# Performance work log

Measured on AMD Instinct MI355X. Metric: run time of the kernel, lower is better.

The kernel has to match this reference:

```python
import jax, jax.numpy as jnp
import numpy as np

N, IN_DIM, HID, HEADS, OUT_DIM = 50000, 128, 32, 4, 64
E, P = 800000, 500000
BN_EPS = 1e-5
NEG_SLOPE = 0.2


def setup_inputs() -> dict:
    key = jax.random.key(0)
    ks = jax.random.split(key, 16)
    inp = {
        "x": jax.random.normal(ks[0], (N, IN_DIM), jnp.float32),
        "ei": jax.random.randint(ks[1], (2, E), 0, N, jnp.int64),
        "src": jax.random.randint(ks[2], (P,), 0, N, jnp.int64),
        "dst": jax.random.randint(ks[3], (P,), 0, N, jnp.int64),
        # conv1: in_dim -> hidden, heads=4, concat
        "W1": jax.random.normal(ks[4], (IN_DIM, HEADS * HID), jnp.float32) * 0.1,
        "a1s": jax.random.normal(ks[5], (HEADS, HID), jnp.float32) * 0.1,
        "a1d": jax.random.normal(ks[6], (HEADS, HID), jnp.float32) * 0.1,
        "b1": jnp.zeros((HEADS * HID,), jnp.float32),
        "bn1_g": jnp.ones((HEADS * HID,), jnp.float32),
        "bn1_b": jnp.zeros((HEADS * HID,), jnp.float32),
        "bn1_m": jnp.zeros((HEADS * HID,), jnp.float32),
        "bn1_v": jnp.ones((HEADS * HID,), jnp.float32),
        # conv2: hidden*heads -> out_dim, heads=1, no concat
        "W2": jax.random.normal(ks[7], (HEADS * HID, OUT_DIM), jnp.float32) * 0.1,
        "a2s": jax.random.normal(ks[8], (1, OUT_DIM), jnp.float32) * 0.1,
        "a2d": jax.random.normal(ks[9], (1, OUT_DIM), jnp.float32) * 0.1,
        "b2": jnp.zeros((OUT_DIM,), jnp.float32),
        "bn2_g": jnp.ones((OUT_DIM,), jnp.float32),
        "bn2_b": jnp.zeros((OUT_DIM,), jnp.float32),
        "bn2_m": jnp.zeros((OUT_DIM,), jnp.float32),
        "bn2_v": jnp.ones((OUT_DIM,), jnp.float32),
        # head MLP: Linear(2*out_dim, out_dim) -> ELU -> Linear(out_dim, 1) -> Sigmoid
        "hW1": jax.random.normal(ks[10], (2 * OUT_DIM, OUT_DIM), jnp.float32) * 0.1,
        "hb1": jnp.zeros((OUT_DIM,), jnp.float32),
        "hW2": jax.random.normal(ks[11], (OUT_DIM, 1), jnp.float32) * 0.1,
        "hb2": jnp.zeros((1,), jnp.float32),
    }
    return inp


def gat_conv(x, e_src, e_dst, W, a_src, a_dst, bias, heads, out_dim, concat):
    # x: [N, F_in]; edges (with self-loops): e_src/e_dst [E']
    n = x.shape[0]
    h = (x @ W).reshape(n, heads, out_dim)            # [N, H, D]
    as_n = jnp.sum(h * a_src, axis=-1)                # [N, H]
    ad_n = jnp.sum(h * a_dst, axis=-1)                # [N, H]
    alpha = jax.nn.leaky_relu(as_n[e_src] + ad_n[e_dst], NEG_SLOPE)  # [E', H]
    # segment softmax over destination nodes
    m = jax.ops.segment_max(alpha, e_dst, num_segments=n)
    m = jnp.where(jnp.isfinite(m), m, 0.0)
    e = jnp.exp(alpha - m[e_dst])
    s = jax.ops.segment_sum(e, e_dst, num_segments=n)
    coef = e / (s[e_dst] + 1e-16)                     # [E', H]
    agg = jax.ops.segment_sum(h[e_src] * coef[:, :, None], e_dst, num_segments=n)
    out = agg.reshape(n, heads * out_dim) if concat else agg.mean(axis=1)
    return out + bias


def batch_norm(x, g, b, m, v):
    return (x - m) * jax.lax.rsqrt(v + BN_EPS) * g + b


def reference(x, ei, src, dst, W1, a1s, a1d, b1, bn1_g, bn1_b, bn1_m, bn1_v,
              W2, a2s, a2d, b2, bn2_g, bn2_b, bn2_m, bn2_v, hW1, hb1, hW2, hb2):
    n = x.shape[0]
    # PyG GATConv default add_self_loops=True
    loops = jnp.arange(n, dtype=ei.dtype)
    e_src = jnp.concatenate([ei[0], loops])
    e_dst = jnp.concatenate([ei[1], loops])

    z = gat_conv(x, e_src, e_dst, W1, a1s, a1d, b1, HEADS, HID, True)
    z = jax.nn.elu(batch_norm(z, bn1_g, bn1_b, bn1_m, bn1_v))
    z = gat_conv(z, e_src, e_dst, W2, a2s, a2d, b2, 1, OUT_DIM, False)
    z = jax.nn.elu(batch_norm(z, bn2_g, bn2_b, bn2_m, bn2_v))

    pair = jnp.concatenate([z[src], z[dst]], axis=1)  # [P, 2*out_dim]
    hidden = jax.nn.elu(pair @ hW1 + hb1)
    logits = hidden @ hW2 + hb2                       # [P, 1]
    return jax.nn.sigmoid(logits).squeeze(-1)
```

## Files before the change

kernel.cpp:

```cpp
#include <hip/hip_runtime.h>
#include <hip/hip_fp16.h>
#include <cmath>

#define HEADS 4
#define HID 32
#define IN_DIM 128
#define OUT_DIM 64
#define D1 (HEADS*HID)
#define NEG_SLOPE 0.2f
#define BN_EPS 1e-5f

__device__ __forceinline__ float2 h2f2(unsigned u) {
  return __half22float2(*reinterpret_cast<const __half2*>(&u));
}


__global__ void deg_count(const int* __restrict__ ei, int E, unsigned* __restrict__ deg)
{
  int e = blockIdx.x*blockDim.x + threadIdx.x;
  if (e < E) atomicAdd(&deg[ei[E + e]], 1u);
}

__global__ void tile_sum(const unsigned* __restrict__ deg, unsigned* __restrict__ part, int n)
{
  __shared__ unsigned red[256];
  int tid = threadIdx.x;
  int i = blockIdx.x*256 + tid;
  red[tid] = (i < n) ? deg[i] + 1u : 0u;
  __syncthreads();
  for (int o = 128; o >= 1; o >>= 1) {
    if (tid < o) red[tid] += red[tid + o];
    __syncthreads();
  }
  if (tid == 0) part[blockIdx.x] = red[0];
}

__global__ void part_scan(unsigned* __restrict__ part, unsigned* __restrict__ offs_n, int ntiles)
{
  __shared__ unsigned sh[256];
  int tid = threadIdx.x;
  unsigned carry = 0;
  for (int base = 0; base < ntiles; base += 256) {
    int i = base + tid;
    unsigned v = (i < ntiles) ? part[i] : 0u;
    sh[tid] = v;
    __syncthreads();
    for (int o = 1; o < 256; o <<= 1) {
      unsigned t = (tid >= o) ? sh[tid - o] : 0u;
      __syncthreads();
      sh[tid] += t;
      __syncthreads();
    }
    unsigned incl = sh[tid];
    if (i < ntiles) part[i] = carry + incl - v;
    unsigned tot = sh[255];
    __syncthreads();
    carry += tot;
  }
  if (tid == 0) offs_n[0] = carry;
}

__global__ void tile_scan_write(const unsigned* __restrict__ deg, const unsigned* __restrict__ part,
                                unsigned* __restrict__ offs, int n)
{
  __shared__ unsigned sh[256];
  int tid = threadIdx.x;
  int i = blockIdx.x*256 + tid;
  unsigned v = (i < n) ? deg[i] + 1u : 0u;
  sh[tid] = v;
  __syncthreads();
  for (int o = 1; o < 256; o <<= 1) {
    unsigned t = (tid >= o) ? sh[tid - o] : 0u;
    __syncthreads();
    sh[tid] += t;
    __syncthreads();
  }
  if (i < n) offs[i] = part[blockIdx.x] + sh[tid] - v;
}

__global__ void csr_fill(const int* __restrict__ ei, int E, int n,
                         const unsigned* __restrict__ offs, unsigned* __restrict__ cursor,
                         int* __restrict__ csr)
{
  int t = blockIdx.x*blockDim.x + threadIdx.x;
  if (t >= E + n) return;
  int s_, d_;
  if (t < E) { s_ = ei[t]; d_ = ei[E + t]; } else { s_ = d_ = t - E; }
  unsigned pos = offs[d_] + atomicAdd(&cursor[d_], 1u);
  csr[pos] = s_;
}

__global__ void prep_wa(const float* __restrict__ W2, const float* __restrict__ a2s,
                        const float* __restrict__ a2d,
                        float* __restrict__ wa_s, float* __restrict__ wa_d)
{
  int k = threadIdx.x;
  float s = 0.f, d = 0.f;
  for (int j = 0; j < OUT_DIM; ++j) {
    float w = W2[k*OUT_DIM + j];
    s = fmaf(w, a2s[j], s);
    d = fmaf(w, a2d[j], d);
  }
  wa_s[k] = s; wa_d[k] = d;
}


__global__ void gemm1(const float* __restrict__ x, const float* __restrict__ W,
                      const float* __restrict__ a_s, const float* __restrict__ a_d,
                      __half2* __restrict__ h, float* __restrict__ asn,
                      float* __restrict__ adn, int n)
{
  __shared__ float xt[IN_DIM][65];
  int tid = threadIdx.x;
  int base = blockIdx.x * 64;
  for (int idx = tid; idx < 64*IN_DIM; idx += 256) {
    int node = idx >> 7, k = idx & 127;
    int gn = base + node;
    xt[k][node] = (gn < n) ? x[(size_t)gn*IN_DIM + k] : 0.f;
  }
  __syncthreads();
  int ng = tid & 7, cg = tid >> 3;
  int n0 = ng * 8, c0 = cg * 4;
  float acc[8][4];
  #pragma unroll
  for (int i = 0; i < 8; ++i) { acc[i][0]=0.f; acc[i][1]=0.f; acc[i][2]=0.f; acc[i][3]=0.f; }
  for (int k = 0; k < IN_DIM; ++k) {
    float4 w = *(const float4*)(W + k*D1 + c0);
    float2 z01 = *(const float2*)&xt[k][n0];
    float2 z23 = *(const float2*)&xt[k][n0+2];
    float2 z45 = *(const float2*)&xt[k][n0+4];
    float2 z67 = *(const float2*)&xt[k][n0+6];
    float zz0=z01.x, zz1=z01.y, zz2=z23.x, zz3=z23.y, zz4=z45.x, zz5=z45.y, zz6=z67.x, zz7=z67.y;
    acc[0][0]=fmaf(zz0,w.x,acc[0][0]); acc[0][1]=fmaf(zz0,w.y,acc[0][1]); acc[0][2]=fmaf(zz0,w.z,acc[0][2]); acc[0][3]=fmaf(zz0,w.w,acc[0][3]);
    acc[1][0]=fmaf(zz1,w.x,acc[1][0]); acc[1][1]=fmaf(zz1,w.y,acc[1][1]); acc[1][2]=fmaf(zz1,w.z,acc[1][2]); acc[1][3]=fmaf(zz1,w.w,acc[1][3]);
    acc[2][0]=fmaf(zz2,w.x,acc[2][0]); acc[2][1]=fmaf(zz2,w.y,acc[2][1]); acc[2][2]=fmaf(zz2,w.z,acc[2][2]); acc[2][3]=fmaf(zz2,w.w,acc[2][3]);
    acc[3][0]=fmaf(zz3,w.x,acc[3][0]); acc[3][1]=fmaf(zz3,w.y,acc[3][1]); acc[3][2]=fmaf(zz3,w.z,acc[3][2]); acc[3][3]=fmaf(zz3,w.w,acc[3][3]);
    acc[4][0]=fmaf(zz4,w.x,acc[4][0]); acc[4][1]=fmaf(zz4,w.y,acc[4][1]); acc[4][2]=fmaf(zz4,w.z,acc[4][2]); acc[4][3]=fmaf(zz4,w.w,acc[4][3]);
    acc[5][0]=fmaf(zz5,w.x,acc[5][0]); acc[5][1]=fmaf(zz5,w.y,acc[5][1]); acc[5][2]=fmaf(zz5,w.z,acc[5][2]); acc[5][3]=fmaf(zz5,w.w,acc[5][3]);
    acc[6][0]=fmaf(zz6,w.x,acc[6][0]); acc[6][1]=fmaf(zz6,w.y,acc[6][1]); acc[6][2]=fmaf(zz6,w.z,acc[6][2]); acc[6][3]=fmaf(zz6,w.w,acc[6][3]);
    acc[7][0]=fmaf(zz7,w.x,acc[7][0]); acc[7][1]=fmaf(zz7,w.y,acc[7][1]); acc[7][2]=fmaf(zz7,w.z,acc[7][2]); acc[7][3]=fmaf(zz7,w.w,acc[7][3]);
  }
  #pragma unroll
  for (int i = 0; i < 8; ++i) {
    int gn = base + n0 + i;
    if (gn >= n) break;
    uint2 pk;
    *reinterpret_cast<__half2*>(&pk.x) = __floats2half2_rn(acc[i][0], acc[i][1]);
    *reinterpret_cast<__half2*>(&pk.y) = __floats2half2_rn(acc[i][2], acc[i][3]);
    *reinterpret_cast<uint2*>(&h[(size_t)gn*64 + cg*2]) = pk;
  }
  float4 asv = *(const float4*)(a_s + c0);
  float4 adv = *(const float4*)(a_d + c0);
  float ps[8], pd[8];
  #pragma unroll
  for (int i = 0; i < 8; ++i) {
    ps[i] = acc[i][0]*asv.x + acc[i][1]*asv.y + acc[i][2]*asv.z + acc[i][3]*asv.w;
    pd[i] = acc[i][0]*adv.x + acc[i][1]*adv.y + acc[i][2]*adv.z + acc[i][3]*adv.w;
  }
  #pragma unroll
  for (int o = 8; o <= 32; o <<= 1) {
    #pragma unroll
    for (int i = 0; i < 8; ++i) { ps[i] += __shfl_xor(ps[i], o); pd[i] += __shfl_xor(pd[i], o); }
  }
  if (((tid & 63) & 56) == 0) {
    int head = tid >> 6;
    #pragma unroll
    for (int i = 0; i < 8; ++i) {
      int gn = base + n0 + i;
      if (gn >= n) break;
      asn[gn*HEADS + head] = ps[i];
      adn[gn*HEADS + head] = pd[i];
    }
  }
}

__global__ void gemm2(const float* __restrict__ z, const float* __restrict__ W,
                      __half2* __restrict__ h2, int n)
{
  __shared__ float zt[D1][65];
  int tid = threadIdx.x;
  int base = blockIdx.x * 64;
  for (int idx = tid; idx < 64*D1; idx += 256) {
    int node = idx >> 7, k = idx & 127;
    int gn = base + node;
    zt[k][node] = (gn < n) ? z[(size_t)gn*D1 + k] : 0.f;
  }
  __syncthreads();
  int ng = tid & 7, cg = tid >> 3;
  int n0 = ng * 8, c0 = cg * 2;
  float a0[8], a1[8];
  #pragma unroll
  for (int i = 0; i < 8; ++i) { a0[i]=0.f; a1[i]=0.f; }
  for (int k = 0; k < D1; ++k) {
    float2 w = *(const float2*)(W + k*OUT_DIM + c0);
    float2 z01 = *(const float2*)&zt[k][n0];
    float2 z23 = *(const float2*)&zt[k][n0+2];
    float2 z45 = *(const float2*)&zt[k][n0+4];
    float2 z67 = *(const float2*)&zt[k][n0+6];
    a0[0]=fmaf(z01.x,w.x,a0[0]); a1[0]=fmaf(z01.x,w.y,a1[0]);
    a0[1]=fmaf(z01.y,w.x,a0[1]); a1[1]=fmaf(z01.y,w.y,a1[1]);
    a0[2]=fmaf(z23.x,w.x,a0[2]); a1[2]=fmaf(z23.x,w.y,a1[2]);
    a0[3]=fmaf(z23.y,w.x,a0[3]); a1[3]=fmaf(z23.y,w.y,a1[3]);
    a0[4]=fmaf(z45.x,w.x,a0[4]); a1[4]=fmaf(z45.x,w.y,a1[4]);
    a0[5]=fmaf(z45.y,w.x,a0[5]); a1[5]=fmaf(z45.y,w.y,a1[5]);
    a0[6]=fmaf(z67.x,w.x,a0[6]); a1[6]=fmaf(z67.x,w.y,a1[6]);
    a0[7]=fmaf(z67.y,w.x,a0[7]); a1[7]=fmaf(z67.y,w.y,a1[7]);
  }
  #pragma unroll
  for (int i = 0; i < 8; ++i) {
    int gn = base + n0 + i;
    if (gn >= n) break;
    h2[(size_t)gn*32 + cg] = __floats2half2_rn(a0[i], a1[i]);
  }
}


__global__ void node_agg1(const int* __restrict__ csr, const unsigned* __restrict__ offs,
                          const float* __restrict__ as1, const float4* __restrict__ ad4,
                          const uint2* __restrict__ hp4, float4* __restrict__ z1out,
                          const float4* __restrict__ b1p, const float4* __restrict__ gp,
                          const float4* __restrict__ bp, const float4* __restrict__ mmp,
                          const float4* __restrict__ vvp,
                          const float4* __restrict__ wa_s4, const float4* __restrict__ wa_d4,
                          float* __restrict__ as2out, float* __restrict__ ad2out, int n)
{
  int lane = threadIdx.x & 63;
  int node = blockIdx.x*4 + (threadIdx.x >> 6);
  if (node >= n) return;
  unsigned beg = offs[node], end = offs[node+1];
  int head = lane >> 4, sub = lane & 15;
  int h = lane >> 5, g = lane & 31;
  int lbase = (g >> 3) * 16;
  float4 advv = ad4[node];
  float adv = head==0 ? advv.x : head==1 ? advv.y : head==2 ? advv.z : advv.w;
  float a0=0.f, a1=0.f, a2=0.f, a3=0.f, s=0.f;
  for (unsigned c = beg; c < end; c += 16) {
    unsigned j = c + sub;
    bool valid = (j < end);
    int sj = valid ? csr[j] : 0;
    float al = as1[sj*HEADS + head] + adv;
    al = al > 0.f ? al : NEG_SLOPE*al;
    float w = valid ? __expf(al) : 0.f;
    float t = w;
    #pragma unroll
    for (int o = 8; o >= 1; o >>= 1) t += __shfl_xor(t, o);
    s += t;
    #pragma unroll
    for (int j2 = 0; j2 < 8; ++j2) {
      int k = j2*2 + h;
      float wv = __shfl(w,  lbase + k);
      int   sv = __shfl(sj, k);
      uint2 hv = hp4[(size_t)sv*32 + g];
      float2 p0 = h2f2(hv.x), p1 = h2f2(hv.y);
      a0 = fmaf(p0.x, wv, a0); a1 = fmaf(p0.y, wv, a1);
      a2 = fmaf(p1.x, wv, a2); a3 = fmaf(p1.y, wv, a3);
    }
  }
  a0 += __shfl_xor(a0, 32); a1 += __shfl_xor(a1, 32);
  a2 += __shfl_xor(a2, 32); a3 += __shfl_xor(a3, 32);
  float sc = __shfl(s, lbase);
  float inv = 1.f / (sc + 1e-16f);
  a0 *= inv; a1 *= inv; a2 *= inv; a3 *= inv;
  if (h == 0) {
    float4 bb = b1p[g], gg = gp[g], be = bp[g], mm = mmp[g], vv = vvp[g];
    float v0 = a0 + bb.x; v0 = (v0 - mm.x) * rsqrtf(vv.x + BN_EPS) * gg.x + be.x;
    float v1 = a1 + bb.y; v1 = (v1 - mm.y) * rsqrtf(vv.y + BN_EPS) * gg.y + be.y;
    float v2 = a2 + bb.z; v2 = (v2 - mm.z) * rsqrtf(vv.z + BN_EPS) * gg.z + be.z;
    float v3 = a3 + bb.w; v3 = (v3 - mm.w) * rsqrtf(vv.w + BN_EPS) * gg.w + be.w;
    v0 = v0 > 0.f ? v0 : expm1f(v0);
    v1 = v1 > 0.f ? v1 : expm1f(v1);
    v2 = v2 > 0.f ? v2 : expm1f(v2);
    v3 = v3 > 0.f ? v3 : expm1f(v3);
    z1out[(size_t)node*32 + g] = make_float4(v0, v1, v2, v3);
    float4 wsv = wa_s4[g], wdv = wa_d4[g];
    float ps = v0*wsv.x + v1*wsv.y + v2*wsv.z + v3*wsv.w;
    float pd = v0*wdv.x + v1*wdv.y + v2*wdv.z + v3*wdv.w;
    #pragma unroll
    for (int o = 16; o >= 1; o >>= 1) { ps += __shfl_xor(ps, o); pd += __shfl_xor(pd, o); }
    if (g == 0) { as2out[node] = ps; ad2out[node] = pd; }
  }
}

__global__ void node_agg2(const int* __restrict__ csr, const unsigned* __restrict__ offs,
                          const float* __restrict__ as2, const float* __restrict__ ad2,
                          const uint2* __restrict__ hp4,
                          const float4* __restrict__ biasp, const float4* __restrict__ gp,
                          const float4* __restrict__ bp, const float4* __restrict__ bmp,
                          const float4* __restrict__ bvp,
                          float4* __restrict__ z2out, int n)
{
  int lane = threadIdx.x & 63;
  int node = blockIdx.x*4 + (threadIdx.x >> 6);
  if (node >= n) return;
  unsigned beg = offs[node], end = offs[node+1];
  int q = lane >> 4, g = lane & 15;
  int sub = lane & 15;
  float adv = ad2[node];
  float a0=0.f, a1=0.f, a2=0.f, a3=0.f, s=0.f;
  for (unsigned c = beg; c < end; c += 16) {
    unsigned j = c + sub;
    bool valid = (j < end);
    int sj = valid ? csr[j] : 0;
    float al = as2[sj] + adv;
    al = al > 0.f ? al : NEG_SLOPE*al;
    float w = valid ? __expf(al) : 0.f;
    float t = w;
    #pragma unroll
    for (int o = 8; o >= 1; o >>= 1) t += __shfl_xor(t, o);
    s += t;
    #pragma unroll
    for (int j2 = 0; j2 < 4; ++j2) {
      int k = j2*4 + q;
      float wv = __shfl(w,  k);
      int   sv = __shfl(sj, k);
      uint2 hv = hp4[(size_t)sv*16 + g];
      float2 p0 = h2f2(hv.x), p1 = h2f2(hv.y);
      a0 = fmaf(p0.x, wv, a0); a1 = fmaf(p0.y, wv, a1);
      a2 = fmaf(p1.x, wv, a2); a3 = fmaf(p1.y, wv, a3);
    }
  }
  a0 += __shfl_xor(a0, 32); a1 += __shfl_xor(a1, 32);
  a2 += __shfl_xor(a2, 32); a3 += __shfl_xor(a3, 32);
  a0 += __shfl_xor(a0, 16); a1 += __shfl_xor(a1, 16);
  a2 += __shfl_xor(a2, 16); a3 += __shfl_xor(a3, 16);
  float inv = 1.f / (s + 1e-16f);
  if (q == 0) {
    float4 bb = biasp[g], gg = gp[g], be = bp[g], mm = bmp[g], vv = bvp[g];
    float v0 = a0*inv + bb.x; v0 = (v0 - mm.x) * rsqrtf(vv.x + BN_EPS) * gg.x + be.x;
    float v1 = a1*inv + bb.y; v1 = (v1 - mm.y) * rsqrtf(vv.y + BN_EPS) * gg.y + be.y;
    float v2 = a2*inv + bb.z; v2 = (v2 - mm.z) * rsqrtf(vv.z + BN_EPS) * gg.z + be.z;
    float v3 = a3*inv + bb.w; v3 = (v3 - mm.w) * rsqrtf(vv.w + BN_EPS) * gg.w + be.w;
    v0 = v0 > 0.f ? v0 : expm1f(v0);
    v1 = v1 > 0.f ? v1 : expm1f(v1);
    v2 = v2 > 0.f ? v2 : expm1f(v2);
    v3 = v3 > 0.f ? v3 : expm1f(v3);
    z2out[(size_t)node*16 + g] = make_float4(v0, v1, v2, v3);
  }
}

__global__ void uv_prep(const float* __restrict__ z2, const float* __restrict__ hW1,
                        __half2* __restrict__ u, __half2* __restrict__ vout, int n)
{
  __shared__ float zt[64][65];
  int tid = threadIdx.x;
  int base = blockIdx.x * 64;
  for (int idx = tid; idx < 64*64; idx += 256) {
    int node = idx >> 6, k = idx & 63;
    int gn = base + node;
    zt[k][node] = (gn < n) ? z2[(size_t)gn*64 + k] : 0.f;
  }
  __syncthreads();
  int ng = tid & 7, cg = tid >> 3;
  int n0 = ng * 8;
  int c0 = (cg & 15) * 4;
  const float* wbase = hW1 + (cg >= 16 ? 64*64 : 0) + c0;
  float acc[8][4];
  #pragma unroll
  for (int i = 0; i < 8; ++i) { acc[i][0]=0.f; acc[i][1]=0.f; acc[i][2]=0.f; acc[i][3]=0.f; }
  for (int k = 0; k < 64; ++k) {
    float4 w = *(const float4*)(wbase + k*64);
    float2 z01 = *(const float2*)&zt[k][n0];
    float2 z23 = *(const float2*)&zt[k][n0+2];
    float2 z45 = *(const float2*)&zt[k][n0+4];
    float2 z67 = *(const float2*)&zt[k][n0+6];
    float zz0=z01.x, zz1=z01.y, zz2=z23.x, zz3=z23.y, zz4=z45.x, zz5=z45.y, zz6=z67.x, zz7=z67.y;
    acc[0][0]=fmaf(zz0,w.x,acc[0][0]); acc[0][1]=fmaf(zz0,w.y,acc[0][1]); acc[0][2]=fmaf(zz0,w.z,acc[0][2]); acc[0][3]=fmaf(zz0,w.w,acc[0][3]);
    acc[1][0]=fmaf(zz1,w.x,acc[1][0]); acc[1][1]=fmaf(zz1,w.y,acc[1][1]); acc[1][2]=fmaf(zz1,w.z,acc[1][2]); acc[1][3]=fmaf(zz1,w.w,acc[1][3]);
    acc[2][0]=fmaf(zz2,w.x,acc[2][0]); acc[2][1]=fmaf(zz2,w.y,acc[2][1]); acc[2][2]=fmaf(zz2,w.z,acc[2][2]); acc[2][3]=fmaf(zz2,w.w,acc[2][3]);
    acc[3][0]=fmaf(zz3,w.x,acc[3][0]); acc[3][1]=fmaf(zz3,w.y,acc[3][1]); acc[3][2]=fmaf(zz3,w.z,acc[3][2]); acc[3][3]=fmaf(zz3,w.w,acc[3][3]);
    acc[4][0]=fmaf(zz4,w.x,acc[4][0]); acc[4][1]=fmaf(zz4,w.y,acc[4][1]); acc[4][2]=fmaf(zz4,w.z,acc[4][2]); acc[4][3]=fmaf(zz4,w.w,acc[4][3]);
    acc[5][0]=fmaf(zz5,w.x,acc[5][0]); acc[5][1]=fmaf(zz5,w.y,acc[5][1]); acc[5][2]=fmaf(zz5,w.z,acc[5][2]); acc[5][3]=fmaf(zz5,w.w,acc[5][3]);
    acc[6][0]=fmaf(zz6,w.x,acc[6][0]); acc[6][1]=fmaf(zz6,w.y,acc[6][1]); acc[6][2]=fmaf(zz6,w.z,acc[6][2]); acc[6][3]=fmaf(zz6,w.w,acc[6][3]);
    acc[7][0]=fmaf(zz7,w.x,acc[7][0]); acc[7][1]=fmaf(zz7,w.y,acc[7][1]); acc[7][2]=fmaf(zz7,w.z,acc[7][2]); acc[7][3]=fmaf(zz7,w.w,acc[7][3]);
  }
  __half2* dst = (cg < 16) ? u : vout;
  int cq = (cg & 15) * 2;
  #pragma unroll
  for (int i = 0; i < 8; ++i) {
    int gn = base + n0 + i;
    if (gn >= n) break;
    uint2 pk;
    *reinterpret_cast<__half2*>(&pk.x) = __floats2half2_rn(acc[i][0], acc[i][1]);
    *reinterpret_cast<__half2*>(&pk.y) = __floats2half2_rn(acc[i][2], acc[i][3]);
    *reinterpret_cast<uint2*>(&dst[(size_t)gn*32 + cq]) = pk;
  }
}

__global__ void pair_score(const int* __restrict__ src, const int* __restrict__ dst,
                           const uint4* __restrict__ u4, const uint4* __restrict__ v4,
                           const float4* __restrict__ hb1, const float4* __restrict__ hW2,
                           const float* __restrict__ hb2, float* __restrict__ out, int P)
{
  int t = blockIdx.x*blockDim.x + threadIdx.x;
  int p = t >> 3, sub = t & 7;
  if (p >= P) return;
  int sp = src[p], dp = dst[p];
  uint4 ua = u4[(size_t)sp*8 + sub];
  uint4 vb = v4[(size_t)dp*8 + sub];
  float4 hbA = hb1[sub*2], hbB = hb1[sub*2+1];
  float4 w2A = hW2[sub*2], w2B = hW2[sub*2+1];
  float2 a0 = h2f2(ua.x), a1 = h2f2(ua.y), a2 = h2f2(ua.z), a3 = h2f2(ua.w);
  float2 b0 = h2f2(vb.x), b1 = h2f2(vb.y), b2 = h2f2(vb.z), b3 = h2f2(vb.w);
  float h0 = a0.x + b0.x + hbA.x; h0 = h0 > 0.f ? h0 : expm1f(h0);
  float h1 = a0.y + b0.y + hbA.y; h1 = h1 > 0.f ? h1 : expm1f(h1);
  float h2 = a1.x + b1.x + hbA.z; h2 = h2 > 0.f ? h2 : expm1f(h2);
  float h3 = a1.y + b1.y + hbA.w; h3 = h3 > 0.f ? h3 : expm1f(h3);
  float h4 = a2.x + b2.x + hbB.x; h4 = h4 > 0.f ? h4 : expm1f(h4);
  float h5 = a2.y + b2.y + hbB.y; h5 = h5 > 0.f ? h5 : expm1f(h5);
  float h6 = a3.x + b3.x + hbB.z; h6 = h6 > 0.f ? h6 : expm1f(h6);
  float h7 = a3.y + b3.y + hbB.w; h7 = h7 > 0.f ? h7 : expm1f(h7);
  float pl = h0*w2A.x + h1*w2A.y + h2*w2A.z + h3*w2A.w
           + h4*w2B.x + h5*w2B.y + h6*w2B.z + h7*w2B.w;
  pl += __shfl_xor(pl, 1);
  pl += __shfl_xor(pl, 2);
  pl += __shfl_xor(pl, 4);
  if (sub == 0) out[p] = 1.f / (1.f + __expf(-(pl + hb2[0])));
}

extern "C" void kernel_launch(void* const* d_in, const int* in_sizes, int n_in,
                              void* d_out, int out_size, void* d_ws, size_t ws_size,
                              hipStream_t stream)
{
  const float* x    = (const float*)d_in[0];
  const int*   ei   = (const int*)d_in[1];
  const int*   src  = (const int*)d_in[2];
  const int*   dst  = (const int*)d_in[3];
  const float* W1   = (const float*)d_in[4];
  const float* a1s  = (const float*)d_in[5];
  const float* a1d  = (const float*)d_in[6];
  const float* b1   = (const float*)d_in[7];
  const float* bn1g = (const float*)d_in[8];
  const float* bn1b = (const float*)d_in[9];
  const float* bn1m = (const float*)d_in[10];
  const float* bn1v = (const float*)d_in[11];
  const float* W2   = (const float*)d_in[12];
  const float* a2s  = (const float*)d_in[13];
  const float* a2d  = (const float*)d_in[14];
  const float* b2   = (const float*)d_in[15];
  const float* bn2g = (const float*)d_in[16];
  const float* bn2b = (const float*)d_in[17];
  const float* bn2m = (const float*)d_in[18];
  const float* bn2v = (const float*)d_in[19];
  const float* hW1  = (const float*)d_in[20];
  const float* hb1  = (const float*)d_in[21];
  const float* hW2  = (const float*)d_in[22];
  const float* hb2  = (const float*)d_in[23];

  const int N  = in_sizes[0] / IN_DIM;
  const int E  = in_sizes[1] / 2;
  const int P  = in_sizes[2];
  const int Ep = E + N;
  const int ntiles = (N + 255) / 256;

  float* ws = (float*)d_ws;
  float* h1   = ws;
  float* z1   = h1 + (size_t)N*D1;
  float* as1  = z1 + (size_t)N*D1;
  float* ad1  = as1 + (size_t)N*HEADS;
  float* as2  = ad1 + (size_t)N*HEADS;
  float* ad2  = as2 + N;
  unsigned* deg    = (unsigned*)(ad2 + N);
  unsigned* offs   = deg + N;
  unsigned* cursor = offs + N + 1;
  unsigned* part   = cursor + N;
  int* csr         = (int*)(part + ntiles);
  float* wa_s      = (float*)(csr + Ep);
  float* wa_d      = wa_s + D1;

  __half2* h1h = (__half2*)h1;
  __half2* h2h = (__half2*)h1;
  float*   z2  = h1 + (size_t)N*OUT_DIM;
  __half2* uh  = (__half2*)z1;
  __half2* vh  = uh + (size_t)N*32;

  hipMemsetAsync(deg,    0, (size_t)N*sizeof(unsigned), stream);
  hipMemsetAsync(cursor, 0, (size_t)N*sizeof(unsigned), stream);
  prep_wa<<<1, 128, 0, stream>>>(W2, a2s, a2d, wa_s, wa_d);
  deg_count<<<(E + 255)/256, 256, 0, stream>>>(ei, E, deg);
  tile_sum<<<ntiles, 256, 0, stream>>>(deg, part, N);
  part_scan<<<1, 256, 0, stream>>>(part, offs + N, ntiles);
  tile_scan_write<<<ntiles, 256, 0, stream>>>(deg, part, offs, N);
  csr_fill<<<(Ep + 255)/256, 256, 0, stream>>>(ei, E, N, offs, cursor, csr);

  gemm1<<<(N + 63)/64, 256, 0, stream>>>(x, W1, a1s, a1d, h1h, as1, ad1, N);
  node_agg1<<<(N + 3)/4, 256, 0, stream>>>(csr, offs, as1, (const float4*)ad1,
                                           (const uint2*)h1h, (float4*)z1,
                                           (const float4*)b1, (const float4*)bn1g,
                                           (const float4*)bn1b, (const float4*)bn1m,
                                           (const float4*)bn1v,
                                           (const float4*)wa_s, (const float4*)wa_d,
                                           as2, ad2, N);

  gemm2<<<(N + 63)/64, 256, 0, stream>>>(z1, W2, h2h, N);
  node_agg2<<<(N + 3)/4, 256, 0, stream>>>(csr, offs, as2, ad2, (const uint2*)h2h,
                                           (const float4*)b2, (const float4*)bn2g,
                                           (const float4*)bn2b, (const float4*)bn2m,
                                           (const float4*)bn2v, (float4*)z2, N);
  uv_prep<<<(N + 63)/64, 256, 0, stream>>>(z2, hW1, uh, vh, N);

  {
    long long total = (long long)P * 8;
    int blocks = (int)((total + 255) / 256);
    pair_score<<<blocks, 256, 0, stream>>>(src, dst, (const uint4*)uh, (const uint4*)vh,
                                           (const float4*)hb1, (const float4*)hW2,
                                           hb2, (float*)d_out, P);
  }
}
```

Measured before the change: 310.0 us.

## Build CSR via two-level bucket sort and halve gemm1 node tile

Replaces the per-edge global-atomic CSR fill with a two-pass bucket sort. Edges are first scattered into buckets of 64 destinations, then each block fills its bucket's CSR slots using shared-memory atomics, which is meant to reduce global atomic contention and improve write locality. gemm1 also moves from 64 to 32 nodes per block, doubling the block count for better occupancy and parallelism at the cost of less weight reuse per block. The new scheme adds an intermediate pairs buffer, extra launches including a serial single-block scan, and makes the order of sources within each row nondeterministic.

```diff
diff --git a/kernel.cpp b/kernel.cpp
--- a/kernel.cpp
+++ b/kernel.cpp
@@ -9,16 +9,76 @@
 #define D1 (HEADS*HID)
 #define NEG_SLOPE 0.2f
 #define BN_EPS 1e-5f
+#define BSHIFT 6
 
 __device__ __forceinline__ float2 h2f2(unsigned u) {
   return __half22float2(*reinterpret_cast<const __half2*>(&u));
 }
 
 
-__global__ void deg_count(const int* __restrict__ ei, int E, unsigned* __restrict__ deg)
-{
-  int e = blockIdx.x*blockDim.x + threadIdx.x;
-  if (e < E) atomicAdd(&deg[ei[E + e]], 1u);
+__global__ void bucket_count(const int* __restrict__ ei, int E, int n,
+                             unsigned* __restrict__ deg, unsigned* __restrict__ bcnt)
+{
+  int t = blockIdx.x*blockDim.x + threadIdx.x;
+  if (t >= E + n) return;
+  int d_;
+  if (t < E) { d_ = ei[E + t]; atomicAdd(&deg[d_], 1u); }
+  else d_ = t - E;
+  atomicAdd(&bcnt[d_ >> BSHIFT], 1u);
+}
+
+__global__ void bucket_scan(unsigned* __restrict__ bcnt, int nb)
+{
+  __shared__ unsigned sh[256];
+  int tid = threadIdx.x;
+  unsigned carry = 0;
+  for (int base = 0; base < nb; base += 256) {
+    int i = base + tid;
+    unsigned v = (i < nb) ? bcnt[i] : 0u;
+    sh[tid] = v;
+    __syncthreads();
+    for (int o = 1; o < 256; o <<= 1) {
+      unsigned t = (tid >= o) ? sh[tid - o] : 0u;
+      __syncthreads();
+      sh[tid] += t;
+      __syncthreads();
+    }
+    if (i < nb) bcnt[i] = carry + sh[tid] - v;
+    unsigned tot = sh[255];
+    __syncthreads();
+    carry += tot;
+  }
+}
+
+__global__ void bucket_scatter(const int* __restrict__ ei, int E, int n,
+                               const unsigned* __restrict__ boffs, unsigned* __restrict__ bcur,
+                               int2* __restrict__ pairs)
+{
+  int t = blockIdx.x*blockDim.x + threadIdx.x;
+  if (t >= E + n) return;
+  int s_, d_;
+  if (t < E) { s_ = ei[t]; d_ = ei[E + t]; } else { s_ = d_ = t - E; }
+  int b = d_ >> BSHIFT;
+  unsigned pos = boffs[b] + atomicAdd(&bcur[b], 1u);
+  pairs[pos] = make_int2(s_, d_);
+}
+
+__global__ void bucket_fill(const int2* __restrict__ pairs, const unsigned* __restrict__ boffs,
+                            const unsigned* __restrict__ offs, int* __restrict__ csr,
+                            int nb, int total)
+{
+  __shared__ unsigned curs[64];
+  int b = blockIdx.x;
+  int tid = threadIdx.x;
+  if (tid < 64) curs[tid] = 0u;
+  __syncthreads();
+  unsigned pb = boffs[b];
+  unsigned pe = (b + 1 < nb) ? boffs[b+1] : (unsigned)total;
+  for (unsigned i = pb + tid; i < pe; i += blockDim.x) {
+    int2 pr = pairs[i];
+    unsigned rank = atomicAdd(&curs[pr.y & 63], 1u);
+    csr[offs[pr.y] + rank] = pr.x;
+  }
 }
 
 __global__ void tile_sum(const unsigned* __restrict__ deg, unsigned* __restrict__ part, int n)
@@ -78,18 +138,6 @@
   if (i < n) offs[i] = part[blockIdx.x] + sh[tid] - v;
 }
 
-__global__ void csr_fill(const int* __restrict__ ei, int E, int n,
-                         const unsigned* __restrict__ offs, unsigned* __restrict__ cursor,
-                         int* __restrict__ csr)
-{
-  int t = blockIdx.x*blockDim.x + threadIdx.x;
-  if (t >= E + n) return;
-  int s_, d_;
-  if (t < E) { s_ = ei[t]; d_ = ei[E + t]; } else { s_ = d_ = t - E; }
-  unsigned pos = offs[d_] + atomicAdd(&cursor[d_], 1u);
-  csr[pos] = s_;
-}
-
 __global__ void prep_wa(const float* __restrict__ W2, const float* __restrict__ a2s,
                         const float* __restrict__ a2d,
                         float* __restrict__ wa_s, float* __restrict__ wa_d)
@@ -110,38 +158,32 @@
                       __half2* __restrict__ h, float* __restrict__ asn,
                       float* __restrict__ adn, int n)
 {
-  __shared__ float xt[IN_DIM][65];
-  int tid = threadIdx.x;
-  int base = blockIdx.x * 64;
-  for (int idx = tid; idx < 64*IN_DIM; idx += 256) {
+  __shared__ float xt[IN_DIM][33];
+  int tid = threadIdx.x;
+  int base = blockIdx.x * 32;
+  for (int idx = tid; idx < 32*IN_DIM; idx += 256) {
     int node = idx >> 7, k = idx & 127;
     int gn = base + node;
     xt[k][node] = (gn < n) ? x[(size_t)gn*IN_DIM + k] : 0.f;
   }
   __syncthreads();
   int ng = tid & 7, cg = tid >> 3;
-  int n0 = ng * 8, c0 = cg * 4;
-  float acc[8][4];
-  #pragma unroll
-  for (int i = 0; i < 8; ++i) { acc[i][0]=0.f; acc[i][1]=0.f; acc[i][2]=0.f; acc[i][3]=0.f; }
+  int n0 = ng * 4, c0 = cg * 4;
+  float acc[4][4];
+  #pragma unroll
+  for (int i = 0; i < 4; ++i) { acc[i][0]=0.f; acc[i][1]=0.f; acc[i][2]=0.f; acc[i][3]=0.f; }
   for (int k = 0; k < IN_DIM; ++k) {
     float4 w = *(const float4*)(W + k*D1 + c0);
     float2 z01 = *(const float2*)&xt[k][n0];
     float2 z23 = *(const float2*)&xt[k][n0+2];
-    float2 z45 = *(const float2*)&xt[k][n0+4];
-    float2 z67 = *(const float2*)&xt[k][n0+6];
-    float zz0=z01.x, zz1=z01.y, zz2=z23.x, zz3=z23.y, zz4=z45.x, zz5=z45.y, zz6=z67.x, zz7=z67.y;
+    float zz0=z01.x, zz1=z01.y, zz2=z23.x, zz3=z23.y;
     acc[0][0]=fmaf(zz0,w.x,acc[0][0]); acc[0][1]=fmaf(zz0,w.y,acc[0][1]); acc[0][2]=fmaf(zz0,w.z,acc[0][2]); acc[0][3]=fmaf(zz0,w.w,acc[0][3]);
     acc[1][0]=fmaf(zz1,w.x,acc[1][0]); acc[1][1]=fmaf(zz1,w.y,acc[1][1]); acc[1][2]=fmaf(zz1,w.z,acc[1][2]); acc[1][3]=fmaf(zz1,w.w,acc[1][3]);
     acc[2][0]=fmaf(zz2,w.x,acc[2][0]); acc[2][1]=fmaf(zz2,w.y,acc[2][1]); acc[2][2]=fmaf(zz2,w.z,acc[2][2]); acc[2][3]=fmaf(zz2,w.w,acc[2][3]);
     acc[3][0]=fmaf(zz3,w.x,acc[3][0]); acc[3][1]=fmaf(zz3,w.y,acc[3][1]); acc[3][2]=fmaf(zz3,w.z,acc[3][2]); acc[3][3]=fmaf(zz3,w.w,acc[3][3]);
-    acc[4][0]=fmaf(zz4,w.x,acc[4][0]); acc[4][1]=fmaf(zz4,w.y,acc[4][1]); acc[4][2]=fmaf(zz4,w.z,acc[4][2]); acc[4][3]=fmaf(zz4,w.w,acc[4][3]);
-    acc[5][0]=fmaf(zz5,w.x,acc[5][0]); acc[5][1]=fmaf(zz5,w.y,acc[5][1]); acc[5][2]=fmaf(zz5,w.z,acc[5][2]); acc[5][3]=fmaf(zz5,w.w,acc[5][3]);
-    acc[6][0]=fmaf(zz6,w.x,acc[6][0]); acc[6][1]=fmaf(zz6,w.y,acc[6][1]); acc[6][2]=fmaf(zz6,w.z,acc[6][2]); acc[6][3]=fmaf(zz6,w.w,acc[6][3]);
-    acc[7][0]=fmaf(zz7,w.x,acc[7][0]); acc[7][1]=fmaf(zz7,w.y,acc[7][1]); acc[7][2]=fmaf(zz7,w.z,acc[7][2]); acc[7][3]=fmaf(zz7,w.w,acc[7][3]);
-  }
-  #pragma unroll
-  for (int i = 0; i < 8; ++i) {
+  }
+  #pragma unroll
+  for (int i = 0; i < 4; ++i) {
     int gn = base + n0 + i;
     if (gn >= n) break;
     uint2 pk;
@@ -151,21 +193,21 @@
   }
   float4 asv = *(const float4*)(a_s + c0);
   float4 adv = *(const float4*)(a_d + c0);
-  float ps[8], pd[8];
-  #pragma unroll
-  for (int i = 0; i < 8; ++i) {
+  float ps[4], pd[4];
+  #pragma unroll
+  for (int i = 0; i < 4; ++i) {
     ps[i] = acc[i][0]*asv.x + acc[i][1]*asv.y + acc[i][2]*asv.z + acc[i][3]*asv.w;
     pd[i] = acc[i][0]*adv.x + acc[i][1]*adv.y + acc[i][2]*adv.z + acc[i][3]*adv.w;
   }
   #pragma unroll
   for (int o = 8; o <= 32; o <<= 1) {
     #pragma unroll
-    for (int i = 0; i < 8; ++i) { ps[i] += __shfl_xor(ps[i], o); pd[i] += __shfl_xor(pd[i], o); }
+    for (int i = 0; i < 4; ++i) { ps[i] += __shfl_xor(ps[i], o); pd[i] += __shfl_xor(pd[i], o); }
   }
   if (((tid & 63) & 56) == 0) {
     int head = tid >> 6;
     #pragma unroll
-    for (int i = 0; i < 8; ++i) {
+    for (int i = 0; i < 4; ++i) {
       int gn = base + n0 + i;
       if (gn >= n) break;
       asn[gn*HEADS + head] = ps[i];
@@ -451,6 +493,7 @@
   const int P  = in_sizes[2];
   const int Ep = E + N;
   const int ntiles = (N + 255) / 256;
+  const int nb = (N + (1 << BSHIFT) - 1) >> BSHIFT;
 
   float* ws = (float*)d_ws;
   float* h1   = ws;
@@ -461,11 +504,13 @@
   float* ad2  = as2 + N;
   unsigned* deg    = (unsigned*)(ad2 + N);
   unsigned* offs   = deg + N;
-  unsigned* cursor = offs + N + 1;
-  unsigned* part   = cursor + N;
-  int* csr         = (int*)(part + ntiles);
-  float* wa_s      = (float*)(csr + Ep);
+  unsigned* part   = offs + N + 2;
+  unsigned* bcnt   = part + ntiles;
+  unsigned* bcur   = bcnt + nb;
+  float* wa_s      = (float*)(bcur + nb);
   float* wa_d      = wa_s + D1;
+  int* csr         = (int*)(wa_d + D1);
+  int2* pairs      = (int2*)(csr + Ep + (Ep & 1));
 
   __half2* h1h = (__half2*)h1;
   __half2* h2h = (__half2*)h1;
@@ -473,16 +518,19 @@
   __half2* uh  = (__half2*)z1;
   __half2* vh  = uh + (size_t)N*32;
 
-  hipMemsetAsync(deg,    0, (size_t)N*sizeof(unsigned), stream);
-  hipMemsetAsync(cursor, 0, (size_t)N*sizeof(unsigned), stream);
+  hipMemsetAsync(deg,  0, (size_t)N*sizeof(unsigned), stream);
+  hipMemsetAsync(bcnt, 0, (size_t)nb*sizeof(unsigned), stream);
+  hipMemsetAsync(bcur, 0, (size_t)nb*sizeof(unsigned), stream);
   prep_wa<<<1, 128, 0, stream>>>(W2, a2s, a2d, wa_s, wa_d);
-  deg_count<<<(E + 255)/256, 256, 0, stream>>>(ei, E, deg);
+  bucket_count<<<(Ep + 255)/256, 256, 0, stream>>>(ei, E, N, deg, bcnt);
+  bucket_scan<<<1, 256, 0, stream>>>(bcnt, nb);
   tile_sum<<<ntiles, 256, 0, stream>>>(deg, part, N);
   part_scan<<<1, 256, 0, stream>>>(part, offs + N, ntiles);
   tile_scan_write<<<ntiles, 256, 0, stream>>>(deg, part, offs, N);
-  csr_fill<<<(Ep + 255)/256, 256, 0, stream>>>(ei, E, N, offs, cursor, csr);
-
-  gemm1<<<(N + 63)/64, 256, 0, stream>>>(x, W1, a1s, a1d, h1h, as1, ad1, N);
+  bucket_scatter<<<(Ep + 255)/256, 256, 0, stream>>>(ei, E, N, bcnt, bcur, pairs);
+  bucket_fill<<<nb, 256, 0, stream>>>(pairs, bcnt, offs, csr, nb, Ep);
+
+  gemm1<<<(N + 31)/32, 256, 0, stream>>>(x, W1, a1s, a1d, h1h, as1, ad1, N);
   node_agg1<<<(N + 3)/4, 256, 0, stream>>>(csr, offs, as1, (const float4*)ad1,
                                            (const uint2*)h1h, (float4*)z1,
                                            (const float4*)b1, (const float4*)bn1g,
```

New measurement: 892.1 us. 2.88x slower.
